# Kernel tuning notes

Hardware: AMD Instinct MI355X
Metric: run time of the kernel (lower is better)

Reference implementation:

```python
import jax, jax.numpy as jnp
import numpy as np

EPS = 1e-7  # K.epsilon()


def setup_inputs() -> dict:
    key = jax.random.key(0)
    k1, k2, k3 = jax.random.split(key, 3)
    B, H, W, Cin, Cout, KH, KW = 8, 128, 128, 256, 256, 3, 3
    x = jax.random.normal(k1, (B, H, W, Cin), dtype=jnp.float32)
    style = jax.random.normal(k2, (B, Cin), dtype=jnp.float32)
    # he_uniform-ish scale for the kernel
    fan_in = KH * KW * Cin
    limit = np.sqrt(6.0 / fan_in)
    kernel = jax.random.uniform(k3, (KH, KW, Cin, Cout), dtype=jnp.float32,
                                minval=-limit, maxval=limit)
    return {"x": x, "style": style, "kernel": kernel}


def reference(x, style, kernel):
    # Demodulation factor: rsqrt(sum_{kh,kw,cin} (kernel * style)^2 + eps), shape (B, Cout).
    # Equivalent to the original's broadcast-then-reduce, computed without
    # materializing the (B,kh,kw,Cin,Cout) modulated weight tensor.
    k2 = jnp.sum(jnp.square(kernel), axis=(0, 1))          # (Cin, Cout)
    ssq = jnp.einsum('io,bi->bo', k2, jnp.square(style))   # (B, Cout)
    demod = jax.lax.rsqrt(ssq + EPS)                       # (B, Cout)

    # Modulate input per-sample, then shared-weight conv (same padding, stride 1).
    xm = x * style[:, None, None, :]                       # (B,H,W,Cin)
    y = jax.lax.conv_general_dilated(
        xm, kernel,
        window_strides=(1, 1), padding='SAME',
        dimension_numbers=('NHWC', 'HWIO', 'NHWC'))
    return y * demod[:, None, None, :]
```

## Files before the change

kernel.cpp:

```cpp
#include <hip/hip_runtime.h>
#include <hip/hip_bf16.h>
#include <stdint.h>

typedef short short8 __attribute__((ext_vector_type(8)));
typedef float f32x4 __attribute__((ext_vector_type(4)));

#define PXS 40

__device__ __forceinline__ short f2bf(float f) {
    __hip_bfloat16 h = __float2bfloat16(f);
    return __builtin_bit_cast(short, h);
}

__global__ void prep_k2(const float* __restrict__ kern, float* __restrict__ K2)
{
    const int ci = blockIdx.x, co = threadIdx.x;
    float acc = 0.f;
#pragma unroll
    for (int p = 0; p < 9; ++p) {
        float w = kern[(p * 256 + ci) * 256 + co];
        acc += w * w;
    }
    K2[ci * 256 + co] = acc;
}

__global__ void prep_demod(const float* __restrict__ style,
                           const float* __restrict__ K2,
                           float* __restrict__ demod)
{
    const int b = blockIdx.x, co = threadIdx.x;
    __shared__ float s2[256];
    float s = style[b * 256 + co];
    s2[co] = s * s;
    __syncthreads();
    float acc = 0.f;
#pragma unroll 8
    for (int ci = 0; ci < 256; ++ci)
        acc += s2[ci] * K2[ci * 256 + co];
    demod[b * 256 + co] = 1.0f / sqrtf(acc + 1e-7f);
}

__global__ void prep_kf(const float* __restrict__ kern,
                        __hip_bfloat16* __restrict__ kf)
{
    const int st = blockIdx.x;
    const int sl = st / 3, tp = st - sl * 3;
    const int dh = sl >> 3, cc = sl & 7;
    const int p  = dh * 3 + tp;
    const int t    = threadIdx.x;
    const int lane = t & 63, jt2 = t >> 6;
    const int l15  = lane & 15, lk = lane >> 4;
    const int cib  = cc * 32 + lk * 8;
#pragma unroll
    for (int jj = 0; jj < 4; ++jj) {
        const int jt = jj * 4 + jt2;
        const int co = jt * 16 + l15;
        short8 v;
#pragma unroll
        for (int e = 0; e < 8; ++e)
            v[e] = f2bf(kern[(size_t)(p * 256 + cib + e) * 256 + co]);
        *(short8*)(kf + ((size_t)(st * 16 + jt) * 64 + lane) * 8) = v;
    }
}

__global__ __launch_bounds__(256) void conv_mfma(
    const float* __restrict__ x,
    const __hip_bfloat16* __restrict__ kf,
    const float* __restrict__ style,
    const float* __restrict__ demod,
    float* __restrict__ out)
{
    __shared__ __align__(16) __hip_bfloat16 Xs[2][130 * PXS];
    __shared__ float Ss[256];
    __shared__ float Ds[128];

    const int t    = threadIdx.x;
    const int bid  = blockIdx.x;
    const int L    = ((bid & 7) << 8) | (bid >> 3);
    const int n0   = (L & 1) << 7;
    const int bh   = L >> 1;
    const int b    = bh >> 7, h = bh & 127;
    const int wave = t >> 6, lane = t & 63;
    const int wr   = (wave >> 1) << 6;
    const int wc   = (wave & 1) << 6;
    const int l15  = lane & 15, lk = lane >> 4;
    const int mA   = t >> 2;
    const int koff = (t & 3) << 3;
    const int jbase = ((L & 1) << 3) + (wc >> 4);

    if (t < 128) {
        ((float2*)Ss)[t] = ((const float2*)(style + b * 256))[t];
        Ds[t] = demod[b * 256 + n0 + t];
    }
    if (t < 32) {
        const __hip_bfloat16 z = __float2bfloat16(0.f);
        Xs[0][t] = z; Xs[0][129 * PXS + t] = z;
        Xs[1][t] = z; Xs[1][129 * PXS + t] = z;
    }

    f32x4 acc[4][4] = {};

    const int slo = (h == 0)   ? 8  : 0;
    const int shi = (h == 127) ? 16 : 24;

    __syncthreads();

    {
        const int h2  = h + (slo >> 3) - 1;
        const int ci0 = (slo & 7) << 5;
        const size_t rowbase = (size_t)(b * 128 + h2) * 128;
        const float* ga = x + (rowbase + mA)      * 256 + ci0 + koff;
        const float* gb = x + (rowbase + mA + 64) * 256 + ci0 + koff;
        float4 xa0 = *(const float4*)ga, xa1 = *(const float4*)(ga + 4);
        float4 xb0 = *(const float4*)gb, xb1 = *(const float4*)(gb + 4);
        float4 s0  = *(const float4*)&Ss[ci0 + koff];
        float4 s1  = *(const float4*)&Ss[ci0 + koff + 4];
        short8 ma, mb;
#pragma unroll
        for (int jj = 0; jj < 4; ++jj) {
            ma[jj]     = f2bf((&xa0.x)[jj] * (&s0.x)[jj]);
            ma[jj + 4] = f2bf((&xa1.x)[jj] * (&s1.x)[jj]);
            mb[jj]     = f2bf((&xb0.x)[jj] * (&s0.x)[jj]);
            mb[jj + 4] = f2bf((&xb1.x)[jj] * (&s1.x)[jj]);
        }
        *(short8*)&Xs[0][(mA + 1)  * PXS + koff] = ma;
        *(short8*)&Xs[0][(mA + 65) * PXS + koff] = mb;
    }
    __syncthreads();

    int cur = 0;
    for (int s = slo; s < shi; ++s, cur ^= 1) {
        float4 xa0, xa1, xb0, xb1;
        int nci0 = 0;
        const bool pf = (s + 1 < shi);
        if (pf) {
            const int sl = s + 1;
            const int h2 = h + (sl >> 3) - 1;
            nci0 = (sl & 7) << 5;
            const size_t rowbase = (size_t)(b * 128 + h2) * 128;
            const float* ga = x + (rowbase + mA)      * 256 + nci0 + koff;
            const float* gb = x + (rowbase + mA + 64) * 256 + nci0 + koff;
            xa0 = *(const float4*)ga; xa1 = *(const float4*)(ga + 4);
            xb0 = *(const float4*)gb; xb1 = *(const float4*)(gb + 4);
        }

        const size_t stbase = (size_t)s * 3 * 16;
#pragma unroll
        for (int tp = 0; tp < 3; ++tp) {
            short8 bfr[4], af[4];
#pragma unroll
            for (int j = 0; j < 4; ++j)
                bfr[j] = *(const short8*)(kf +
                    (((stbase + tp * 16) + jbase + j) * 64 + lane) * 8);
#pragma unroll
            for (int i = 0; i < 4; ++i)
                af[i] = *(const short8*)&Xs[cur][(wr + i * 16 + l15 + tp) * PXS + lk * 8];
#pragma unroll
            for (int i = 0; i < 4; ++i)
#pragma unroll
                for (int j = 0; j < 4; ++j)
                    acc[i][j] = __builtin_amdgcn_mfma_f32_16x16x32_bf16(
                        af[i], bfr[j], acc[i][j], 0, 0, 0);
        }

        if (pf) {
            float4 s0 = *(const float4*)&Ss[nci0 + koff];
            float4 s1 = *(const float4*)&Ss[nci0 + koff + 4];
            short8 ma, mb;
#pragma unroll
            for (int jj = 0; jj < 4; ++jj) {
                ma[jj]     = f2bf((&xa0.x)[jj] * (&s0.x)[jj]);
                ma[jj + 4] = f2bf((&xa1.x)[jj] * (&s1.x)[jj]);
                mb[jj]     = f2bf((&xb0.x)[jj] * (&s0.x)[jj]);
                mb[jj + 4] = f2bf((&xb1.x)[jj] * (&s1.x)[jj]);
            }
            *(short8*)&Xs[cur ^ 1][(mA + 1)  * PXS + koff] = ma;
            *(short8*)&Xs[cur ^ 1][(mA + 65) * PXS + koff] = mb;
        }
        __syncthreads();
    }

    float dj[4];
#pragma unroll
    for (int j = 0; j < 4; ++j) dj[j] = Ds[wc + j * 16 + l15];
    const size_t obase = (size_t)(b * 128 + h) * 128 * 256 + n0;
#pragma unroll
    for (int i = 0; i < 4; ++i) {
#pragma unroll
        for (int j = 0; j < 4; ++j) {
            const int n = wc + j * 16 + l15;
#pragma unroll
            for (int r = 0; r < 4; ++r) {
                const int m = wr + i * 16 + lk * 4 + r;
                out[obase + (size_t)m * 256 + n] = acc[i][j][r] * dj[j];
            }
        }
    }
}

extern "C" void kernel_launch(void* const* d_in, const int* in_sizes, int n_in,
                              void* d_out, int out_size, void* d_ws, size_t ws_size,
                              hipStream_t stream)
{
    const float* x     = (const float*)d_in[0];
    const float* style = (const float*)d_in[1];
    const float* kern  = (const float*)d_in[2];
    float* out = (float*)d_out;

    char*  ws    = (char*)d_ws;
    float* demod = (float*)ws;
    float* K2    = (float*)(ws + 8192);
    __hip_bfloat16* kT = (__hip_bfloat16*)(ws + 270336);

    prep_k2   <<<256, 256, 0, stream>>>(kern, K2);
    prep_demod<<<8,   256, 0, stream>>>(style, K2, demod);
    prep_kf   <<<72,  256, 0, stream>>>(kern, kT);
    conv_mfma <<<2048, 256, 0, stream>>>(x, kT, style, demod, out);
}
```

Baseline: 368.9 us.

## Software-pipeline tap fragment loads ahead of MFMAs and use nontemporal output stores

Restructures the per-slice inner loop so the A/B fragments for the next tap are loaded before the current tap's MFMAs, double-buffering registers across the three taps, and issues the global prefetch of the next x slice after that. It also sets launch_bounds to request 3 blocks per CU and switches output writes to nontemporal stores to avoid polluting cache. The goal is to hide global weight and LDS load latency behind MFMA work. The extra live registers from the double buffering may conflict with the occupancy bound and cause spills.

```diff
diff --git a/kernel.cpp b/kernel.cpp
--- a/kernel.cpp
+++ b/kernel.cpp
@@ -63,7 +63,33 @@
     }
 }
 
-__global__ __launch_bounds__(256) void conv_mfma(
+__device__ __forceinline__ void load_tap(const __hip_bfloat16* __restrict__ kf,
+                                         const __hip_bfloat16* __restrict__ Xrow,
+                                         int sbase, int tp, int jbase, int lane,
+                                         int wr, int l15, int lk,
+                                         short8 af[4], short8 bfr[4])
+{
+#pragma unroll
+    for (int j = 0; j < 4; ++j)
+        bfr[j] = *(const short8*)(kf +
+            (size_t)(sbase + tp * 16 + jbase + j) * 512 + lane * 8);
+#pragma unroll
+    for (int i = 0; i < 4; ++i)
+        af[i] = *(const short8*)&Xrow[(wr + i * 16 + l15 + tp) * PXS + lk * 8];
+}
+
+__device__ __forceinline__ void mfma_tap(f32x4 acc[4][4],
+                                         const short8 af[4], const short8 bfr[4])
+{
+#pragma unroll
+    for (int i = 0; i < 4; ++i)
+#pragma unroll
+        for (int j = 0; j < 4; ++j)
+            acc[i][j] = __builtin_amdgcn_mfma_f32_16x16x32_bf16(
+                af[i], bfr[j], acc[i][j], 0, 0, 0);
+}
+
+__global__ __launch_bounds__(256, 3) void conv_mfma(
     const float* __restrict__ x,
     const __hip_bfloat16* __restrict__ kf,
     const float* __restrict__ style,
@@ -86,7 +112,7 @@
     const int l15  = lane & 15, lk = lane >> 4;
     const int mA   = t >> 2;
     const int koff = (t & 3) << 3;
-    const int jbase = ((L & 1) << 3) + (wc >> 4);
+    const int jbase = ((L & 1) << 3) + ((wave & 1) << 2);
 
     if (t < 128) {
         ((float2*)Ss)[t] = ((const float2*)(style + b * 256))[t];
@@ -130,6 +156,17 @@
 
     int cur = 0;
     for (int s = slo; s < shi; ++s, cur ^= 1) {
+        const int sbase = s * 48;
+        const __hip_bfloat16* Xr = Xs[cur];
+
+        short8 afA[4], bfA[4], afB[4], bfB[4];
+        load_tap(kf, Xr, sbase, 0, jbase, lane, wr, l15, lk, afA, bfA);
+        load_tap(kf, Xr, sbase, 1, jbase, lane, wr, l15, lk, afB, bfB);
+
+        mfma_tap(acc, afA, bfA);
+
+        load_tap(kf, Xr, sbase, 2, jbase, lane, wr, l15, lk, afA, bfA);
+
         float4 xa0, xa1, xb0, xb1;
         int nci0 = 0;
         const bool pf = (s + 1 < shi);
@@ -144,24 +181,8 @@
             xb0 = *(const float4*)gb; xb1 = *(const float4*)(gb + 4);
         }
 
-        const size_t stbase = (size_t)s * 3 * 16;
-#pragma unroll
-        for (int tp = 0; tp < 3; ++tp) {
-            short8 bfr[4], af[4];
-#pragma unroll
-            for (int j = 0; j < 4; ++j)
-                bfr[j] = *(const short8*)(kf +
-                    (((stbase + tp * 16) + jbase + j) * 64 + lane) * 8);
-#pragma unroll
-            for (int i = 0; i < 4; ++i)
-                af[i] = *(const short8*)&Xs[cur][(wr + i * 16 + l15 + tp) * PXS + lk * 8];
-#pragma unroll
-            for (int i = 0; i < 4; ++i)
-#pragma unroll
-                for (int j = 0; j < 4; ++j)
-                    acc[i][j] = __builtin_amdgcn_mfma_f32_16x16x32_bf16(
-                        af[i], bfr[j], acc[i][j], 0, 0, 0);
-        }
+        mfma_tap(acc, afB, bfB);
+        mfma_tap(acc, afA, bfA);
 
         if (pf) {
             float4 s0 = *(const float4*)&Ss[nci0 + koff];
@@ -192,7 +213,8 @@
 #pragma unroll
             for (int r = 0; r < 4; ++r) {
                 const int m = wr + i * 16 + lk * 4 + r;
-                out[obase + (size_t)m * 256 + n] = acc[i][j][r] * dj[j];
+                __builtin_nontemporal_store(acc[i][j][r] * dj[j],
+                                            &out[obase + (size_t)m * 256 + n]);
             }
         }
     }
```

Result: faster. 359.7 us (-2.5%).
